# Kernel optimization log

Measured on AMD Instinct MI355X. Metric: run time of the kernel, lower is better.

## Reference

```python
import math
import jax, jax.numpy as jnp
import numpy as np


def fht(x):
    """Normalized fast Hadamard transform over the last axis (size = power of 2)."""
    n = x.shape[-1]
    pre = x.shape[:-1]
    y = x.reshape(-1, n)
    h = 1
    while h < n:
        y = y.reshape(-1, n // (2 * h), 2, h)
        a = y[:, :, 0, :]
        b = y[:, :, 1, :]
        y = jnp.stack([a + b, a - b], axis=2)
        h *= 2
    return y.reshape(*pre, n) * jnp.float32(1.0 / math.sqrt(n))


def setup_inputs() -> dict:
    key = jax.random.key(0)
    ks = jax.random.split(key, 8)
    B, N, M, G = 8192, 4096, 4096, 512  # tokens, in_features(n_pad), out_features(m_pad), n_pad//8
    CB = 256  # E8 shell codebook entries (8-bit indices), each an 8-dim lattice point
    x = jax.random.normal(ks[0], (B, N), dtype=jnp.float32)
    Qidxs = jax.random.randint(ks[1], (M, G), 0, CB, dtype=jnp.int32)
    Qidxs2 = jax.random.randint(ks[2], (M, G), 0, CB, dtype=jnp.int32)
    SU = jax.random.rademacher(ks[3], (M,), dtype=jnp.float32)  # row sign vector
    SV = jax.random.rademacher(ks[4], (N,), dtype=jnp.float32)  # column sign vector
    codebook = jax.random.normal(ks[5], (CB, 8), dtype=jnp.float32)
    codebook2 = jax.random.normal(ks[6], (CB, 8), dtype=jnp.float32)
    Wscale = jnp.asarray(0.85, dtype=jnp.float32)
    inv_resid_scale = jnp.asarray(0.07, dtype=jnp.float32)  # nonzero -> stage-2 enabled
    return {"x": x, "Qidxs": Qidxs, "Qidxs2": Qidxs2, "SU": SU, "SV": SV,
            "codebook": codebook, "codebook2": codebook2,
            "Wscale": Wscale, "inv_resid_scale": inv_resid_scale}


def reference(x, Qidxs, Qidxs2, SU, SV, codebook, codebook2, Wscale, inv_resid_scale):
    # in_features == n_pad and out_features == m_pad here (powers of 2), so no pad/slice.
    m_pad, g = Qidxs.shape
    n_pad = g * 8
    # 1) input RHT: signs then Hadamard
    x_rht = fht(x * SV[None, :])  # (B, n_pad)
    # 2) dequantize weights in RHT domain: codebook lookup per 8-dim group + residual stage
    W_rht = codebook[Qidxs].reshape(m_pad, n_pad)
    W_rht = W_rht + codebook2[Qidxs2].reshape(m_pad, n_pad) * inv_resid_scale
    # 3) matmul in RHT domain with global scale
    y_rht = (x_rht @ W_rht.T) * Wscale  # (B, m_pad)
    # 4) output inverse RHT: Hadamard then signs
    y = fht(y_rht) * SU[None, :]
    return y
```

## Files before the change

kernel.cpp:

```cpp
#include <hip/hip_runtime.h>

#define B_DIM 8192
#define N_DIM 4096
#define M_DIM 4096
#define G_DIM 512

typedef short bf16x8 __attribute__((ext_vector_type(8)));
typedef float f32x4 __attribute__((ext_vector_type(4)));

typedef __attribute__((address_space(1))) const void gvoid_t;
typedef __attribute__((address_space(3))) void lvoid_t;

__device__ __forceinline__ void load_lds16(const void* g, void* l) {
    __builtin_amdgcn_global_load_lds((gvoid_t*)g, (lvoid_t*)l, 16, 0, 0);
}

__device__ __forceinline__ unsigned lds_u32(const void* p) {
    return (unsigned)(unsigned long long)(lvoid_t*)p;
}

__device__ __forceinline__ unsigned short f2bf(float f) {
    union { float f; unsigned int u; } v; v.f = f;
    unsigned int u = v.u;
    unsigned int r = (u + 0x7fffu + ((u >> 16) & 1u)) >> 16;
    return (unsigned short)r;
}
__device__ __forceinline__ float bf2f(unsigned short s) {
    union { unsigned int u; float f; } v; v.u = ((unsigned int)s) << 16;
    return v.f;
}

__device__ __forceinline__ void h16(float* v) {
#pragma unroll
    for (int h = 1; h < 16; h <<= 1) {
#pragma unroll
        for (int i = 0; i < 16; i++) {
            if (!(i & h)) {
                float a = v[i], b = v[i | h];
                v[i] = a + b;
                v[i | h] = a - b;
            }
        }
    }
}

__device__ __forceinline__ void h64(float* v) {
#pragma unroll
    for (int h = 1; h < 64; h <<= 1) {
#pragma unroll
        for (int i = 0; i < 64; i++) {
            if (!(i & h)) {
                float a = v[i], b = v[i | h];
                v[i] = a + b;
                v[i | h] = a - b;
            }
        }
    }
}

__global__ __launch_bounds__(256) void k_build_w(
    const int* __restrict__ q1, const int* __restrict__ q2,
    const float* __restrict__ cb1, const float* __restrict__ cb2,
    const float* __restrict__ wsp, const float* __restrict__ irsp,
    unsigned short* __restrict__ W) {
    __shared__ float c1[256 * 9];
    __shared__ float c2[256 * 9];
    int t = threadIdx.x;
#pragma unroll
    for (int j = 0; j < 8; j++) {
        c1[t * 9 + j] = cb1[t * 8 + j];
        c2[t * 9 + j] = cb2[t * 8 + j];
    }
    __syncthreads();
    float ws = wsp[0];
    float irs = irsp[0] * ws;
    int gid = blockIdx.x * 256 + t;
    int i1 = q1[gid] * 9;
    int i2 = q2[gid] * 9;
    union { unsigned short s[8]; int4 v; } o;
#pragma unroll
    for (int j = 0; j < 8; j++) {
        o.s[j] = f2bf(c1[i1 + j] * ws + c2[i2 + j] * irs);
    }
    *(int4*)(W + (size_t)gid * 8) = o.v;
}

__global__ __launch_bounds__(256) void k_hadw(
    unsigned short* __restrict__ W, int base_mul, int step, float scale) {
    int c = blockIdx.x * 256 + threadIdx.x;
    int base = blockIdx.y * base_mul;
    float v[64];
#pragma unroll
    for (int j = 0; j < 64; j++)
        v[j] = bf2f(W[(size_t)(base + j * step) * N_DIM + c]);
    h64(v);
#pragma unroll
    for (int j = 0; j < 64; j++)
        W[(size_t)(base + j * step) * N_DIM + c] = f2bf(v[j] * scale);
}

__global__ __launch_bounds__(256) void k_rht_in(
    const float* __restrict__ x, const float* __restrict__ SV,
    unsigned short* __restrict__ out) {
    __shared__ float lds[4352];
    int row = blockIdx.x;
    int t = threadIdx.x;
    const float* xr = x + (size_t)row * N_DIM;
    float v[16];
#pragma unroll
    for (int r = 0; r < 16; r++) {
        int n = t + (r << 8);
        v[r] = xr[n] * SV[n] * 0.015625f;
    }
    h16(v);
#pragma unroll
    for (int r = 0; r < 16; r++) { int n = t + (r << 8); lds[n + (n >> 4)] = v[r]; }
    __syncthreads();
#pragma unroll
    for (int r = 0; r < 16; r++) { int n = (t << 4) + r; v[r] = lds[n + (n >> 4)]; }
    h16(v);
#pragma unroll
    for (int r = 0; r < 16; r++) { int n = (t << 4) + r; lds[n + (n >> 4)] = v[r]; }
    __syncthreads();
#pragma unroll
    for (int r = 0; r < 16; r++) {
        int n = (t & 15) | (r << 4) | ((t >> 4) << 8);
        v[r] = lds[n + (n >> 4)];
    }
    h16(v);
#pragma unroll
    for (int r = 0; r < 16; r++) {
        int n = (t & 15) | (r << 4) | ((t >> 4) << 8);
        lds[n + (n >> 4)] = v[r];
    }
    __syncthreads();
    unsigned short* orow = out + (size_t)row * N_DIM;
#pragma unroll
    for (int r = 0; r < 16; r++) {
        int n = t + (r << 8);
        orow[n] = f2bf(lds[n + (n >> 4)]);
    }
}

#define DSR(D, A, OFF) \
    asm volatile("ds_read_b128 %0, %1 offset:" #OFF : "=v"(D) : "v"(A))

__global__ __launch_bounds__(512, 2) void k_gemm(
    const unsigned short* __restrict__ A,
    const unsigned short* __restrict__ Bw,
    const float* __restrict__ SU,
    float* __restrict__ C) {
    __shared__ __align__(16) unsigned short lds[4 * 16384];

    int t = threadIdx.x;
    int w = t >> 6;
    int l = t & 63;

    int lin = blockIdx.x;
    int xcd = lin & 7;
    int idx = lin >> 3;
    int bn = xcd * 2 + (idx >> 5);
    int bm = idx & 31;

    int lx = l ^ (l >> 3);
    const unsigned short* aS0 =
        A + (size_t)(bm * 256 + w * 16 + (lx >> 2)) * N_DIM + (lx & 3) * 8;
    const unsigned short* aS1 = aS0 + (size_t)128 * N_DIM;
    const unsigned short* bS0 =
        Bw + (size_t)(bn * 256 + w * 16 + (lx >> 2)) * N_DIM + (lx & 3) * 8;
    const unsigned short* bS1 = bS0 + (size_t)128 * N_DIM;

    int wm = w >> 2;
    int wn = w & 3;
    int quad = l >> 4;
    int ln = l & 15;
    unsigned ldsU = lds_u32(lds);
    unsigned aBase = ldsU +
        (unsigned)(((((wm * 128) + ln) << 6) | (quad << 4)) ^ ((ln >> 1) << 4));
    unsigned bBase = ldsU + 16384u +
        (unsigned)(((((wn * 64) + ln) << 6) | (quad << 4)) ^ ((ln >> 1) << 4));

    f32x4 acc[8][4];
#pragma unroll
    for (int i = 0; i < 8; i++)
#pragma unroll
        for (int j = 0; j < 4; j++) {
            f32x4 z = {0.f, 0.f, 0.f, 0.f};
            acc[i][j] = z;
        }

#define STAGE(KT) do {                                              \
        int kt_ = (KT);                                             \
        int ks_ = kt_ < 127 ? kt_ : 127;                            \
        unsigned short* d_ = lds + ((unsigned)kt_ & 3u) * 16384 + w * 512; \
        const unsigned short* sa0_ = aS0 + ks_ * 32;                \
        const unsigned short* sa1_ = aS1 + ks_ * 32;                \
        const unsigned short* sb0_ = bS0 + ks_ * 32;                \
        const unsigned short* sb1_ = bS1 + ks_ * 32;                \
        load_lds16(sa0_, d_);                                       \
        load_lds16(sa1_, d_ + 4096);                                \
        load_lds16(sb0_, d_ + 8192);                                \
        load_lds16(sb1_, d_ + 12288);                               \
    } while (0)

    STAGE(0);
    STAGE(1);
    STAGE(2);

    for (int k = 0; k < N_DIM / 32; k++) {
        asm volatile("s_waitcnt vmcnt(8)");
        __builtin_amdgcn_s_barrier();
        STAGE(k + 3);

        unsigned au = aBase + (unsigned)(k & 3) * 32768u;
        unsigned bu = bBase + (unsigned)(k & 3) * 32768u;
        bf16x8 af[8], bfr[4];
        DSR(af[0], au, 0);
        DSR(af[1], au, 1024);
        DSR(af[2], au, 2048);
        DSR(af[3], au, 3072);
        DSR(af[4], au, 4096);
        DSR(af[5], au, 5120);
        DSR(af[6], au, 6144);
        DSR(af[7], au, 7168);
        DSR(bfr[0], bu, 0);
        DSR(bfr[1], bu, 1024);
        DSR(bfr[2], bu, 2048);
        DSR(bfr[3], bu, 3072);
        asm volatile("s_waitcnt lgkmcnt(0)");
        __builtin_amdgcn_sched_barrier(0);

        __builtin_amdgcn_s_setprio(1);
#pragma unroll
        for (int i = 0; i < 8; i++)
#pragma unroll
            for (int j = 0; j < 4; j++)
                acc[i][j] = __builtin_amdgcn_mfma_f32_16x16x32_bf16(
                    af[i], bfr[j], acc[i][j], 0, 0, 0);
        __builtin_amdgcn_s_setprio(0);
    }
    asm volatile("s_waitcnt vmcnt(0)");

#pragma unroll
    for (int j = 0; j < 4; j++) {
        int col = bn * 256 + wn * 64 + j * 16 + ln;
        float su = SU[col];
#pragma unroll
        for (int i = 0; i < 8; i++) {
#pragma unroll
            for (int r = 0; r < 4; r++) {
                int rowg = bm * 256 + wm * 128 + i * 16 + quad * 4 + r;
                C[(size_t)rowg * M_DIM + col] = acc[i][j][r] * su;
            }
        }
    }
#undef STAGE
}

extern "C" void kernel_launch(void* const* d_in, const int* in_sizes, int n_in,
                              void* d_out, int out_size, void* d_ws, size_t ws_size,
                              hipStream_t stream) {
    const float* x    = (const float*)d_in[0];
    const int*   q1   = (const int*)d_in[1];
    const int*   q2   = (const int*)d_in[2];
    const float* SU   = (const float*)d_in[3];
    const float* SV   = (const float*)d_in[4];
    const float* cb1  = (const float*)d_in[5];
    const float* cb2  = (const float*)d_in[6];
    const float* wsp  = (const float*)d_in[7];
    const float* irsp = (const float*)d_in[8];
    float* out = (float*)d_out;

    unsigned short* xrht = (unsigned short*)d_ws;
    unsigned short* Wb   = xrht + (size_t)B_DIM * N_DIM;

    k_build_w<<<dim3((M_DIM * G_DIM) / 256), dim3(256), 0, stream>>>(
        q1, q2, cb1, cb2, wsp, irsp, Wb);
    k_hadw<<<dim3(N_DIM / 256, 64), dim3(256), 0, stream>>>(Wb, 1, 64, 1.0f);
    k_hadw<<<dim3(N_DIM / 256, 64), dim3(256), 0, stream>>>(Wb, 64, 1, 0.015625f);
    k_rht_in<<<dim3(B_DIM), dim3(256), 0, stream>>>(x, SV, xrht);
    k_gemm<<<dim3(512), dim3(512), 0, stream>>>(xrht, Wb, SU, out);
}
```

Measured before the change: 516.3 us.

## Fuse weight Hadamard passes into one LDS kernel and split GEMM loop into halves

New measurement: 579.9 us. 1.12x slower.

```diff
diff --git a/kernel.cpp b/kernel.cpp
--- a/kernel.cpp
+++ b/kernel.cpp
@@ -85,18 +85,55 @@
     *(int4*)(W + (size_t)gid * 8) = o.v;
 }
 
-__global__ __launch_bounds__(256) void k_hadw(
-    unsigned short* __restrict__ W, int base_mul, int step, float scale) {
-    int c = blockIdx.x * 256 + threadIdx.x;
-    int base = blockIdx.y * base_mul;
+#define HW_S 4160
+__global__ __launch_bounds__(256) void k_hadw2(unsigned short* __restrict__ W) {
+    __shared__ float lds[8 * HW_S];
+    int t = threadIdx.x;
+    int c0 = blockIdx.x * 8;
+#pragma unroll
+    for (int p = 0; p < 16; p++) {
+        int r = t + (p << 8);
+        union { int4 v; unsigned short s[8]; } u;
+        u.v = *(const int4*)(W + (size_t)r * N_DIM + c0);
+        int fr = r + (r >> 6);
+#pragma unroll
+        for (int c = 0; c < 8; c++) lds[c * HW_S + fr] = bf2f(u.s[c]);
+    }
+    __syncthreads();
     float v[64];
 #pragma unroll
-    for (int j = 0; j < 64; j++)
-        v[j] = bf2f(W[(size_t)(base + j * step) * N_DIM + c]);
-    h64(v);
-#pragma unroll
-    for (int j = 0; j < 64; j++)
-        W[(size_t)(base + j * step) * N_DIM + c] = f2bf(v[j] * scale);
+    for (int p = 0; p < 2; p++) {
+        int idx = t + (p << 8);
+        int c = idx >> 6, lo = idx & 63;
+        float* base = &lds[c * HW_S + lo];
+#pragma unroll
+        for (int hi = 0; hi < 64; hi++) v[hi] = base[hi * 65];
+        h64(v);
+#pragma unroll
+        for (int hi = 0; hi < 64; hi++) base[hi * 65] = v[hi];
+    }
+    __syncthreads();
+#pragma unroll
+    for (int p = 0; p < 2; p++) {
+        int idx = t + (p << 8);
+        int c = idx >> 6, hi = idx & 63;
+        float* base = &lds[c * HW_S + hi * 65];
+#pragma unroll
+        for (int lo = 0; lo < 64; lo++) v[lo] = base[lo];
+        h64(v);
+#pragma unroll
+        for (int lo = 0; lo < 64; lo++) base[lo] = v[lo] * 0.015625f;
+    }
+    __syncthreads();
+#pragma unroll
+    for (int p = 0; p < 16; p++) {
+        int r = t + (p << 8);
+        int fr = r + (r >> 6);
+        union { int4 v; unsigned short s[8]; } u;
+#pragma unroll
+        for (int c = 0; c < 8; c++) u.s[c] = f2bf(lds[c * HW_S + fr]);
+        *(int4*)(W + (size_t)r * N_DIM + c0) = u.v;
+    }
 }
 
 __global__ __launch_bounds__(256) void k_rht_in(
@@ -144,6 +181,7 @@
 
 #define DSR(D, A, OFF) \
     asm volatile("ds_read_b128 %0, %1 offset:" #OFF : "=v"(D) : "v"(A))
+#define SB0() __builtin_amdgcn_sched_barrier(0)
 
 __global__ __launch_bounds__(512, 2) void k_gemm(
     const unsigned short* __restrict__ A,
@@ -189,57 +227,73 @@
             acc[i][j] = z;
         }
 
-#define STAGE(KT) do {                                              \
+#define STAGE_A(KT) do {                                            \
         int kt_ = (KT);                                             \
         int ks_ = kt_ < 127 ? kt_ : 127;                            \
         unsigned short* d_ = lds + ((unsigned)kt_ & 3u) * 16384 + w * 512; \
-        const unsigned short* sa0_ = aS0 + ks_ * 32;                \
-        const unsigned short* sa1_ = aS1 + ks_ * 32;                \
-        const unsigned short* sb0_ = bS0 + ks_ * 32;                \
-        const unsigned short* sb1_ = bS1 + ks_ * 32;                \
-        load_lds16(sa0_, d_);                                       \
-        load_lds16(sa1_, d_ + 4096);                                \
-        load_lds16(sb0_, d_ + 8192);                                \
-        load_lds16(sb1_, d_ + 12288);                               \
+        load_lds16(aS0 + ks_ * 32, d_);                             \
+        load_lds16(aS1 + ks_ * 32, d_ + 4096);                      \
     } while (0)
-
-    STAGE(0);
-    STAGE(1);
-    STAGE(2);
-
+#define STAGE_B(KT) do {                                            \
+        int kt_ = (KT);                                             \
+        int ks_ = kt_ < 127 ? kt_ : 127;                            \
+        unsigned short* d_ = lds + ((unsigned)kt_ & 3u) * 16384 + w * 512; \
+        load_lds16(bS0 + ks_ * 32, d_ + 8192);                      \
+        load_lds16(bS1 + ks_ * 32, d_ + 12288);                     \
+    } while (0)
+
+#define GROUP(I) do {                                               \
+        acc[I][0] = __builtin_amdgcn_mfma_f32_16x16x32_bf16(        \
+            af[I], bfr[0], acc[I][0], 0, 0, 0);                     \
+        acc[I][1] = __builtin_amdgcn_mfma_f32_16x16x32_bf16(        \
+            af[I], bfr[1], acc[I][1], 0, 0, 0);                     \
+        acc[I][2] = __builtin_amdgcn_mfma_f32_16x16x32_bf16(        \
+            af[I], bfr[2], acc[I][2], 0, 0, 0);                     \
+        acc[I][3] = __builtin_amdgcn_mfma_f32_16x16x32_bf16(        \
+            af[I], bfr[3], acc[I][3], 0, 0, 0);                     \
+    } while (0)
+
+    STAGE_A(0); STAGE_B(0);
+    STAGE_A(1); STAGE_B(1);
+    STAGE_A(2); STAGE_B(2);
+    asm volatile("s_waitcnt vmcnt(8)");
+    __builtin_amdgcn_s_barrier();
+
+    bf16x8 af[8], bfr[4];
     for (int k = 0; k < N_DIM / 32; k++) {
-        asm volatile("s_waitcnt vmcnt(8)");
-        __builtin_amdgcn_s_barrier();
-        STAGE(k + 3);
-
         unsigned au = aBase + (unsigned)(k & 3) * 32768u;
         unsigned bu = bBase + (unsigned)(k & 3) * 32768u;
-        bf16x8 af[8], bfr[4];
         DSR(af[0], au, 0);
         DSR(af[1], au, 1024);
         DSR(af[2], au, 2048);
         DSR(af[3], au, 3072);
+        DSR(bfr[0], bu, 0);
+        DSR(bfr[1], bu, 1024);
+        DSR(bfr[2], bu, 2048);
+        DSR(bfr[3], bu, 3072);
+        STAGE_A(k + 3);
+        __builtin_amdgcn_s_barrier();
+        asm volatile("s_waitcnt lgkmcnt(0)");
+        SB0();
+        __builtin_amdgcn_s_setprio(1);
+        GROUP(0); GROUP(1); GROUP(2); GROUP(3);
+        __builtin_amdgcn_s_setprio(0);
+        __builtin_amdgcn_s_barrier();
         DSR(af[4], au, 4096);
         DSR(af[5], au, 5120);
         DSR(af[6], au, 6144);
         DSR(af[7], au, 7168);
-        DSR(bfr[0], bu, 0);
-        DSR(bfr[1], bu, 1024);
-        DSR(bfr[2], bu, 2048);
-        DSR(bfr[3], bu, 3072);
+        STAGE_B(k + 3);
+        __builtin_amdgcn_s_barrier();
         asm volatile("s_waitcnt lgkmcnt(0)");
-        __builtin_amdgcn_sched_barrier(0);
-
+        SB0();
         __builtin_amdgcn_s_setprio(1);
-#pragma unroll
-        for (int i = 0; i < 8; i++)
-#pragma unroll
-            for (int j = 0; j < 4; j++)
-                acc[i][j] = __builtin_amdgcn_mfma_f32_16x16x32_bf16(
-                    af[i], bfr[j], acc[i][j], 0, 0, 0);
+        GROUP(4); GROUP(5); GROUP(6); GROUP(7);
         __builtin_amdgcn_s_setprio(0);
-    }
-    asm volatile("s_waitcnt vmcnt(0)");
+        asm volatile("s_waitcnt vmcnt(8)");
+        __builtin_amdgcn_s_barrier();
+    }
+    asm volatile("s_waitcnt vmcnt(0) lgkmcnt(0)");
 
 #pragma unroll
     for (int j = 0; j < 4; j++) {
@@ -254,7 +308,9 @@
             }
         }
     }
-#undef STAGE
+#undef STAGE_A
+#undef STAGE_B
+#undef GROUP
 }
 
 extern "C" void kernel_launch(void* const* d_in, const int* in_sizes, int n_in,
@@ -276,8 +332,7 @@
 
     k_build_w<<<dim3((M_DIM * G_DIM) / 256), dim3(256), 0, stream>>>(
         q1, q2, cb1, cb2, wsp, irsp, Wb);
-    k_hadw<<<dim3(N_DIM / 256, 64), dim3(256), 0, stream>>>(Wb, 1, 64, 1.0f);
-    k_hadw<<<dim3(N_DIM / 256, 64), dim3(256), 0, stream>>>(Wb, 64, 1, 0.015625f);
+    k_hadw2<<<dim3(N_DIM / 8), dim3(256), 0, stream>>>(Wb);
     k_rht_in<<<dim3(B_DIM), dim3(256), 0, stream>>>(x, SV, xrht);
     k_gemm<<<dim3(512), dim3(512), 0, stream>>>(xrht, Wb, SU, out);
 }
```

## Software-pipeline LDS fragment reads with MFMA using double-buffered B registers

Applied to the files above, without the earlier changes.

Result: no change. 521.0 us (+0.9%).

```diff
diff --git a/kernel.cpp b/kernel.cpp
--- a/kernel.cpp
+++ b/kernel.cpp
@@ -144,6 +144,8 @@
 
 #define DSR(D, A, OFF) \
     asm volatile("ds_read_b128 %0, %1 offset:" #OFF : "=v"(D) : "v"(A))
+#define SB0() __builtin_amdgcn_sched_barrier(0)
+#define SGB(M, N) __builtin_amdgcn_sched_group_barrier((M), (N), 0)
 
 __global__ __launch_bounds__(512, 2) void k_gemm(
     const unsigned short* __restrict__ A,
@@ -175,9 +177,9 @@
     int quad = l >> 4;
     int ln = l & 15;
     unsigned ldsU = lds_u32(lds);
-    unsigned aBase = ldsU +
+    unsigned aByte = ldsU +
         (unsigned)(((((wm * 128) + ln) << 6) | (quad << 4)) ^ ((ln >> 1) << 4));
-    unsigned bBase = ldsU + 16384u +
+    unsigned bByte = ldsU + 16384u +
         (unsigned)(((((wn * 64) + ln) << 6) | (quad << 4)) ^ ((ln >> 1) << 4));
 
     f32x4 acc[8][4];
@@ -193,53 +195,82 @@
         int kt_ = (KT);                                             \
         int ks_ = kt_ < 127 ? kt_ : 127;                            \
         unsigned short* d_ = lds + ((unsigned)kt_ & 3u) * 16384 + w * 512; \
-        const unsigned short* sa0_ = aS0 + ks_ * 32;                \
-        const unsigned short* sa1_ = aS1 + ks_ * 32;                \
-        const unsigned short* sb0_ = bS0 + ks_ * 32;                \
-        const unsigned short* sb1_ = bS1 + ks_ * 32;                \
-        load_lds16(sa0_, d_);                                       \
-        load_lds16(sa1_, d_ + 4096);                                \
-        load_lds16(sb0_, d_ + 8192);                                \
-        load_lds16(sb1_, d_ + 12288);                               \
+        load_lds16(aS0 + ks_ * 32, d_);                             \
+        load_lds16(aS1 + ks_ * 32, d_ + 4096);                      \
+        load_lds16(bS0 + ks_ * 32, d_ + 8192);                      \
+        load_lds16(bS1 + ks_ * 32, d_ + 12288);                     \
     } while (0)
+
+#define GROUP(I, BC) do {                                           \
+        acc[I][0] = __builtin_amdgcn_mfma_f32_16x16x32_bf16(        \
+            af[I], BC[0], acc[I][0], 0, 0, 0);                      \
+        acc[I][1] = __builtin_amdgcn_mfma_f32_16x16x32_bf16(        \
+            af[I], BC[1], acc[I][1], 0, 0, 0);                      \
+        acc[I][2] = __builtin_amdgcn_mfma_f32_16x16x32_bf16(        \
+            af[I], BC[2], acc[I][2], 0, 0, 0);                      \
+        acc[I][3] = __builtin_amdgcn_mfma_f32_16x16x32_bf16(        \
+            af[I], BC[3], acc[I][3], 0, 0, 0);                      \
+    } while (0)
+
+#define BODY(K, BC, BN) do {                                        \
+        asm volatile("s_waitcnt lgkmcnt(0)");                       \
+        SB0();   \
+        STAGE((K) + 3);                                             \
+        unsigned aun = aByte + ((unsigned)((K) + 1) & 3u) * 32768u; \
+        unsigned bun = bByte + ((unsigned)((K) + 1) & 3u) * 32768u; \
+        SGB(0x10, 4);                       \
+        GROUP(0, BC); DSR(af[0], aun, 0);    DSR(BN[0], bun, 0);    \
+        SGB(0x8, 4); SGB(0x100, 2);                                 \
+        GROUP(1, BC); DSR(af[1], aun, 1024); DSR(BN[1], bun, 1024); \
+        SGB(0x8, 4); SGB(0x100, 2);                                 \
+        GROUP(2, BC); DSR(af[2], aun, 2048); DSR(BN[2], bun, 2048); \
+        SGB(0x8, 4); SGB(0x100, 2);                                 \
+        GROUP(3, BC); DSR(af[3], aun, 3072); DSR(BN[3], bun, 3072); \
+        SGB(0x8, 4); SGB(0x100, 2);                                 \
+        GROUP(4, BC); DSR(af[4], aun, 4096);                        \
+        SGB(0x8, 4); SGB(0x100, 1);                                 \
+        GROUP(5, BC); DSR(af[5], aun, 5120);                        \
+        SGB(0x8, 4); SGB(0x100, 1);                                 \
+        GROUP(6, BC); DSR(af[6], aun, 6144);                        \
+        SGB(0x8, 4); SGB(0x100, 1);                                 \
+        GROUP(7, BC); DSR(af[7], aun, 7168);                        \
+        SGB(0x8, 4); SGB(0x100, 1);                                 \
+        asm volatile("s_waitcnt vmcnt(4)");   \
+        asm volatile("" ::: "memory");                              \
+        __builtin_amdgcn_s_barrier();                               \
+        asm volatile("" ::: "memory");                              \
+    } while (0)
+
+    bf16x8 af[8], bfrA[4], bfrB[4];
 
     STAGE(0);
     STAGE(1);
     STAGE(2);
-
-    for (int k = 0; k < N_DIM / 32; k++) {
-        asm volatile("s_waitcnt vmcnt(8)");
-        __builtin_amdgcn_s_barrier();
-        STAGE(k + 3);
-
-        unsigned au = aBase + (unsigned)(k & 3) * 32768u;
-        unsigned bu = bBase + (unsigned)(k & 3) * 32768u;
-        bf16x8 af[8], bfr[4];
-        DSR(af[0], au, 0);
-        DSR(af[1], au, 1024);
-        DSR(af[2], au, 2048);
-        DSR(af[3], au, 3072);
-        DSR(af[4], au, 4096);
-        DSR(af[5], au, 5120);
-        DSR(af[6], au, 6144);
-        DSR(af[7], au, 7168);
-        DSR(bfr[0], bu, 0);
-        DSR(bfr[1], bu, 1024);
-        DSR(bfr[2], bu, 2048);
-        DSR(bfr[3], bu, 3072);
-        asm volatile("s_waitcnt lgkmcnt(0)");
-        __builtin_amdgcn_sched_barrier(0);
-
-        __builtin_amdgcn_s_setprio(1);
-#pragma unroll
-        for (int i = 0; i < 8; i++)
-#pragma unroll
-            for (int j = 0; j < 4; j++)
-                acc[i][j] = __builtin_amdgcn_mfma_f32_16x16x32_bf16(
-                    af[i], bfr[j], acc[i][j], 0, 0, 0);
-        __builtin_amdgcn_s_setprio(0);
-    }
-    asm volatile("s_waitcnt vmcnt(0)");
+    asm volatile("s_waitcnt vmcnt(4)");
+    __builtin_amdgcn_s_barrier();
+    asm volatile("" ::: "memory");
+    {
+        unsigned au0 = aByte;
+        unsigned bu0 = bByte;
+        DSR(af[0], au0, 0);
+        DSR(af[1], au0, 1024);
+        DSR(af[2], au0, 2048);
+        DSR(af[3], au0, 3072);
+        DSR(af[4], au0, 4096);
+        DSR(af[5], au0, 5120);
+        DSR(af[6], au0, 6144);
+        DSR(af[7], au0, 7168);
+        DSR(bfrA[0], bu0, 0);
+        DSR(bfrA[1], bu0, 1024);
+        DSR(bfrA[2], bu0, 2048);
+        DSR(bfrA[3], bu0, 3072);
+    }
+
+    for (int k = 0; k < N_DIM / 32; k += 2) {
+        BODY(k, bfrA, bfrB);
+        BODY(k + 1, bfrB, bfrA);
+    }
+    asm volatile("s_waitcnt vmcnt(0) lgkmcnt(0)");
 
 #pragma unroll
     for (int j = 0; j < 4; j++) {
@@ -255,6 +286,8 @@
         }
     }
 #undef STAGE
+#undef GROUP
+#undef BODY
 }
 
 extern "C" void kernel_launch(void* const* d_in, const int* in_sizes, int n_in,
```
